# Kernel optimization log

Measured on AMD Instinct MI355X. Metric: run time of the kernel, lower is better.

The kernel has to match this reference:

```python
import jax, jax.numpy as jnp
from jax import lax
import numpy as np

B, S, D, H, L, DFF = 64, 512, 512, 8, 6, 2048
CLIP_C = 10.0
EPS = 1e-5


def setup_inputs() -> dict:
    key = jax.random.key(0)
    ks = jax.random.split(key, 16)
    sc = 0.02
    inp = {
        "x": jax.random.normal(ks[0], (B, S, D), jnp.float32),
        "mask": jnp.zeros((B, S, S), jnp.float32),
        # stacked per-layer params [L, ...]; Linear stored as (out, in) like torch
        "qkv_w": jax.random.normal(ks[1], (L, 3 * D, D), jnp.float32) * sc,
        "qkv_b": jnp.zeros((L, 3 * D), jnp.float32),
        "ln1_g": jnp.ones((L, D), jnp.float32),
        "ln1_b": jnp.zeros((L, D), jnp.float32),
        "kv_w": jax.random.normal(ks[2], (L, 2 * D, D), jnp.float32) * sc,
        "kv_b": jnp.zeros((L, 2 * D), jnp.float32),
        "ln2_g": jnp.ones((L, D), jnp.float32),
        "ln2_b": jnp.zeros((L, D), jnp.float32),
        "w1": jax.random.normal(ks[3], (L, DFF, D), jnp.float32) * sc,
        "b1": jnp.zeros((L, DFF), jnp.float32),
        "w2": jax.random.normal(ks[4], (L, D, DFF), jnp.float32) * sc,
        "b2": jnp.zeros((L, D), jnp.float32),
        "ln3_g": jnp.ones((L, D), jnp.float32),
        "ln3_b": jnp.zeros((L, D), jnp.float32),
    }
    return inp


def _ln(v, g, b):
    m = v.mean(-1, keepdims=True)
    var = ((v - m) ** 2).mean(-1, keepdims=True)
    return (v - m) * lax.rsqrt(var + EPS) * g + b


def _mha(q, k, v, mask, clip_c):
    # faithful to custom_multi_head_attn: bmm -> /sqrt(hd) -> [c*tanh] -> +mask -> softmax -> bmm
    b, sq, d = q.shape
    sk = k.shape[1]
    hd = d // H
    qh = q.reshape(b, sq, H, hd)
    kh = k.reshape(b, sk, H, hd)
    vh = v.reshape(b, sk, H, hd)
    s = jnp.einsum('bqhd,bkhd->bhqk', qh, kh) * (1.0 / float(hd) ** 0.5)
    if clip_c is not None:
        s = clip_c * jnp.tanh(s)
    if mask is not None:
        s = s + mask[:, None]  # repeat over heads
    a = jax.nn.softmax(s, axis=-1)
    return jnp.einsum('bhqk,bkhd->bqhd', a, vh).reshape(b, sq, d)


def reference(x, mask, qkv_w, qkv_b, ln1_g, ln1_b, kv_w, kv_b, ln2_g, ln2_b,
              w1, b1, w2, b2, ln3_g, ln3_b):
    def step(h, p):
        (qw, qb, g1, be1, kw, kb, g2, be2, fw1, fb1, fw2, fb2, g3, be3) = p
        # self-attention block (no FFN, no mask, no clip; note: NO out-projection,
        # matching the original which never applies out_proj_weight)
        qkv = h @ qw.T + qb
        q, k, v = jnp.split(qkv, 3, axis=-1)
        x1 = _ln(h + _mha(q, k, v, None, None), g1, be1)
        # cross-attention block: query = sa output (no q_proj), kv from original h
        kv_ = h @ kw.T + kb
        k2, v2 = jnp.split(kv_, 2, axis=-1)
        y = _ln(x1 + _mha(x1, k2, v2, mask, CLIP_C), g2, be2)
        # FFN + residual + norm (post-norm)
        ff = jax.nn.relu(y @ fw1.T + fb1) @ fw2.T + fb2
        return _ln(y + ff, g3, be3), None

    params = (qkv_w, qkv_b, ln1_g, ln1_b, kv_w, kv_b, ln2_g, ln2_b,
              w1, b1, w2, b2, ln3_g, ln3_b)
    out, _ = lax.scan(step, x, params)
    return out
```

## Files before the change

kernel.cpp:

```cpp
#include <hip/hip_runtime.h>


typedef __bf16 bf16_t;
typedef __bf16 bf16x8 __attribute__((ext_vector_type(8)));
typedef __bf16 bf16x4 __attribute__((ext_vector_type(4)));
typedef float  f32x4  __attribute__((ext_vector_type(4)));

#define NB   64
#define NS   512
#define ND   512
#define NH   8
#define NHD  64
#define NL   6
#define NDFF 2048
#define NM   (NB * NS)

__device__ __forceinline__ void gld_lds16(const void* gsrc, void* lds) {
  __builtin_amdgcn_global_load_lds((__attribute__((address_space(1))) void*)gsrc,
                                   (__attribute__((address_space(3))) void*)lds,
                                   16, 0, 0);
}

template<int N> __device__ __forceinline__ void vm_wait() {
  if constexpr (N == 0)      asm volatile("s_waitcnt vmcnt(0)" ::: "memory");
  else if constexpr (N == 3) asm volatile("s_waitcnt vmcnt(3)" ::: "memory");
}
__device__ __forceinline__ void lgkm0() {
  asm volatile("s_waitcnt lgkmcnt(0)" ::: "memory");
}

__global__ __launch_bounds__(256) void cvt_f32_bf16(const float* __restrict__ in,
                                                    bf16_t* __restrict__ out,
                                                    long n) {
  long i = ((long)blockIdx.x * 256 + threadIdx.x) * 8;
  const long stride = (long)gridDim.x * 256 * 8;
  for (; i < n; i += stride) {
    f32x4 a = *(const f32x4*)(in + i);
    f32x4 b = *(const f32x4*)(in + i + 4);
    bf16x8 o;
#pragma unroll
    for (int j = 0; j < 4; ++j) { o[j] = (bf16_t)a[j]; o[j + 4] = (bf16_t)b[j]; }
    *(bf16x8*)(out + i) = o;
  }
}

template<bool RELU, bool BIAS_ROW>
__global__ __launch_bounds__(512, 2) void gemm64(const bf16_t* __restrict__ Ap,
                                                 const bf16_t* __restrict__ Wp,
                                                 const float* __restrict__ bias,
                                                 bf16_t* __restrict__ Cout,
                                                 int Nn, int Kk) {
  __shared__ __attribute__((aligned(16))) bf16_t As[2][128 * 32];
  __shared__ __attribute__((aligned(16))) bf16_t Bs[2][256 * 32];
  const int tid = threadIdx.x;
  const int l   = tid & 63;
  const int w   = tid >> 6;
  const int wr  = w >> 2;
  const int wc  = w & 3;
  const int l15 = l & 15, lg = l >> 4;

  const int nn   = Nn >> 8;
  const int nwg  = gridDim.x;
  const int flat = blockIdx.x;
  const int wgid = (nwg & 7) ? flat : (flat & 7) * (nwg >> 3) + (flat >> 3);
  const int m0 = (wgid / nn) * 128;
  const int n0 = (wgid % nn) * 256;

  const int srow = tid >> 2;
  const int sg   = (tid & 3) ^ (srow & 3);

  auto stA = [&](int bf_, int kc) {
    gld_lds16(Ap + (size_t)(m0 + srow) * Kk + kc + sg * 8,
              &As[bf_][(w * 16) * 32]);
  };
  auto stB = [&](int bf_, int p, int kc) {
    gld_lds16(Wp + (size_t)(n0 + p * 128 + srow) * Kk + kc + sg * 8,
              &Bs[bf_][(p * 128 + w * 16) * 32]);
  };
  auto stage = [&](int kt, int bf_) {
    const int kc = kt * 32;
    stA(bf_, kc); stB(bf_, 0, kc); stB(bf_, 1, kc);
  };
  auto ldA = [&](int bf_, int mi) -> bf16x8 {
    const int row = wr * 64 + mi * 16 + l15;
    return *(const bf16x8*)&As[bf_][row * 32 + ((lg ^ (row & 3)) * 8)];
  };
  auto ldB = [&](int bf_, int ni) -> bf16x8 {
    const int row = wc * 64 + ni * 16 + l15;
    return *(const bf16x8*)&Bs[bf_][row * 32 + ((lg ^ (row & 3)) * 8)];
  };

  f32x4 acc[4][4];
#pragma unroll
  for (int i = 0; i < 4; ++i)
#pragma unroll
    for (int j = 0; j < 4; ++j) acc[i][j] = (f32x4){0.f, 0.f, 0.f, 0.f};

  const int KT = Kk >> 5;
  stage(0, 0);
  stage(1, 1);

  for (int kt = 0; kt < KT; ++kt) {
    const int buf = kt & 1;
    if (kt + 1 < KT) vm_wait<3>(); else vm_wait<0>();
    __builtin_amdgcn_s_barrier();

    bf16x8 af[4], bfr[4];
#pragma unroll
    for (int i = 0; i < 4; ++i) { af[i] = ldA(buf, i); bfr[i] = ldB(buf, i); }
    __builtin_amdgcn_s_setprio(1);
#pragma unroll
    for (int mi = 0; mi < 4; ++mi)
#pragma unroll
      for (int ni = 0; ni < 4; ++ni)
        acc[mi][ni] = __builtin_amdgcn_mfma_f32_16x16x32_bf16(af[mi], bfr[ni], acc[mi][ni], 0, 0, 0);
    __builtin_amdgcn_s_setprio(0);

    lgkm0();
    __builtin_amdgcn_s_barrier();
    if (kt + 2 < KT) stage(kt + 2, buf);
  }

#pragma unroll
  for (int mi = 0; mi < 4; ++mi)
#pragma unroll
    for (int ni = 0; ni < 4; ++ni) {
      const int col = n0 + wc * 64 + ni * 16 + l15;
      const float bc = BIAS_ROW ? 0.f : bias[col];
#pragma unroll
      for (int r = 0; r < 4; ++r) {
        const int rowi = m0 + wr * 64 + mi * 16 + lg * 4 + r;
        float v = acc[mi][ni][r] + (BIAS_ROW ? bias[rowi] : bc);
        if (RELU) v = fmaxf(v, 0.f);
        Cout[(size_t)rowi * Nn + col] = (bf16_t)v;
      }
    }
}

template<int CROSS, bool M16>
__global__ __launch_bounds__(256, 2) void attn5(const bf16_t* __restrict__ Q,
                                                const bf16_t* __restrict__ K,
                                                const bf16_t* __restrict__ Vt,
                                                const void* __restrict__ maskp,
                                                bf16_t* __restrict__ O,
                                                int qstride, int kstride, int vstride) {
  __shared__ __attribute__((aligned(16))) bf16_t k_s[2][64 * 64];
  __shared__ __attribute__((aligned(16))) bf16_t v_s[2][64 * 64];
  __shared__ __attribute__((aligned(16))) bf16_t p_s[64 * 64];

  const int tid = threadIdx.x;
  const int l   = tid & 63;
  const int w   = tid >> 6;
  const int bid = blockIdx.x;
  const int h   = bid & 7;
  const int qt  = (bid >> 3) & 7;
  const int b   = bid >> 6;
  const int h64 = h * NHD;
  const int l15 = l & 15, lg = l >> 4;

  const int qglob = qt * 64 + w * 16 + l15;

  auto stageK = [&](int kt, int buf) {
#pragma unroll
    for (int i = 0; i < 2; ++i) {
      const int r  = i * 32 + (tid >> 3);
      const int c8 = (tid & 7) ^ (r & 7);
      gld_lds16(K + (size_t)(b * NS + kt * 64 + r) * kstride + h64 + c8 * 8,
                &k_s[buf][(i * 32 + w * 8) * 64]);
    }
  };
  auto stageV = [&](int kt, int buf) {
#pragma unroll
    for (int i = 0; i < 2; ++i) {
      const int d = i * 32 + (tid >> 3);
      const int g = (tid & 7) ^ (d & 7);
      gld_lds16(Vt + (size_t)(h64 + d) * vstride + b * NS + kt * 64 + g * 8,
                &v_s[buf][(i * 32 + w * 8) * 64]);
    }
  };

  stageK(0, 0); stageV(0, 0);

  bf16x8 qf[2];
#pragma unroll
  for (int c = 0; c < 2; ++c)
    qf[c] = *(const bf16x8*)(Q + (size_t)(b * NS + qglob) * qstride + h64 + c * 32 + lg * 8);

  bf16x4 mk16[2][4];
  f32x4  mkf[2][4];
  if (CROSS) {
#pragma unroll
    for (int nt = 0; nt < 4; ++nt) {
      if (M16) mk16[0][nt] = *(const bf16x4*)((const bf16_t*)maskp
                              + (size_t)(b * NS + qglob) * NS + nt * 16 + lg * 4);
      else     mkf[0][nt]  = *(const f32x4*)((const float*)maskp
                              + (size_t)(b * NS + qglob) * NS + nt * 16 + lg * 4);
    }
  }

  float m_run = -3e38f, l_run = 0.f;
  const f32x4 zz = {0.f, 0.f, 0.f, 0.f};
  f32x4 oacc[4] = {zz, zz, zz, zz};

#pragma unroll
  for (int kt = 0; kt < 8; ++kt) {
    const int buf = kt & 1;
    __syncthreads();
    if (kt < 7) {
      stageK(kt + 1, buf ^ 1);
      stageV(kt + 1, buf ^ 1);
      if (CROSS) {
#pragma unroll
        for (int nt = 0; nt < 4; ++nt) {
          if (M16) mk16[buf ^ 1][nt] = *(const bf16x4*)((const bf16_t*)maskp
                     + (size_t)(b * NS + qglob) * NS + (kt + 1) * 64 + nt * 16 + lg * 4);
          else     mkf[buf ^ 1][nt]  = *(const f32x4*)((const float*)maskp
                     + (size_t)(b * NS + qglob) * NS + (kt + 1) * 64 + nt * 16 + lg * 4);
        }
      }
    }

    f32x4 s[4];
    __builtin_amdgcn_s_setprio(1);
#pragma unroll
    for (int nt = 0; nt < 4; ++nt) {
      const int row = nt * 16 + l15;
      bf16x8 ka0 = *(const bf16x8*)((const char*)k_s[buf] + row * 128 + ((lg ^ (row & 7)) * 16));
      bf16x8 ka1 = *(const bf16x8*)((const char*)k_s[buf] + row * 128 + (((4 + lg) ^ (row & 7)) * 16));
      f32x4 z = zz;
      z = __builtin_amdgcn_mfma_f32_16x16x32_bf16(ka0, qf[0], z, 0, 0, 0);
      z = __builtin_amdgcn_mfma_f32_16x16x32_bf16(ka1, qf[1], z, 0, 0, 0);
      s[nt] = z;
    }
    __builtin_amdgcn_s_setprio(0);

    float tmax = -3e38f;
#pragma unroll
    for (int nt = 0; nt < 4; ++nt) {
      f32x4 v = s[nt] * 0.125f;
      if (CROSS) {
#pragma unroll
        for (int r = 0; r < 4; ++r) {
          const float e2 = __expf(2.f * v[r]);
          const float mkv = M16 ? (float)mk16[buf][nt][r] : mkf[buf][nt][r];
          v[r] = 10.f - 20.f * __builtin_amdgcn_rcpf(e2 + 1.f) + mkv;
        }
      }
      s[nt] = v;
#pragma unroll
      for (int r = 0; r < 4; ++r) tmax = fmaxf(tmax, v[r]);
    }
    tmax = fmaxf(tmax, __shfl_xor(tmax, 16, 64));
    tmax = fmaxf(tmax, __shfl_xor(tmax, 32, 64));
    const float m_new = fmaxf(m_run, tmax);
    const float f = __expf(m_run - m_new);
    float fq[4];
#pragma unroll
    for (int r = 0; r < 4; ++r) fq[r] = __shfl(f, lg * 4 + r, 64);
#pragma unroll
    for (int dt = 0; dt < 4; ++dt)
#pragma unroll
      for (int r = 0; r < 4; ++r) oacc[dt][r] *= fq[r];

    float ts = 0.f;
#pragma unroll
    for (int nt = 0; nt < 4; ++nt) {
      f32x4 v = s[nt];
#pragma unroll
      for (int r = 0; r < 4; ++r) { const float e = __expf(v[r] - m_new); ts += e; v[r] = e; }
      s[nt] = v;
    }
    l_run = l_run * f + ts;
    m_run = m_new;

    const int prow = w * 16 + l15;
#pragma unroll
    for (int nt = 0; nt < 4; ++nt) {
      bf16x4 pk;
#pragma unroll
      for (int r = 0; r < 4; ++r) pk[r] = (bf16_t)s[nt][r];
      const int gran = (nt * 2 + (lg >> 1)) ^ (prow & 7);
      *(bf16x4*)((char*)p_s + prow * 128 + gran * 16 + (lg & 1) * 8) = pk;
    }

    __builtin_amdgcn_s_setprio(1);
#pragma unroll
    for (int ks = 0; ks < 2; ++ks) {
      const int ag = (ks * 4 + lg) ^ (prow & 7);
      bf16x8 pa = *(const bf16x8*)((const char*)p_s + prow * 128 + ag * 16);
#pragma unroll
      for (int dt = 0; dt < 4; ++dt) {
        const int vrow = dt * 16 + l15;
        const int vg   = (ks * 4 + lg) ^ (vrow & 7);
        bf16x8 vb = *(const bf16x8*)((const char*)v_s[buf] + vrow * 128 + vg * 16);
        oacc[dt] = __builtin_amdgcn_mfma_f32_16x16x32_bf16(pa, vb, oacc[dt], 0, 0, 0);
      }
    }
    __builtin_amdgcn_s_setprio(0);
  }

  l_run += __shfl_xor(l_run, 16, 64);
  l_run += __shfl_xor(l_run, 32, 64);
  const float inv = 1.f / l_run;
  float invq[4];
#pragma unroll
  for (int r = 0; r < 4; ++r) invq[r] = __shfl(inv, lg * 4 + r, 64);
#pragma unroll
  for (int dt = 0; dt < 4; ++dt)
#pragma unroll
    for (int r = 0; r < 4; ++r) {
      const size_t row = (size_t)(b * NS + qt * 64 + w * 16 + lg * 4 + r);
      O[row * ND + h64 + dt * 16 + l15] = (bf16_t)(oacc[dt][r] * invq[r]);
    }
}

template<bool A16, bool W32>
__global__ __launch_bounds__(256) void add_ln2(const void* __restrict__ Xav,
                                               const bf16_t* __restrict__ Xb,
                                               const float* __restrict__ gw,
                                               const float* __restrict__ bw,
                                               float* __restrict__ o32,
                                               bf16_t* __restrict__ o16) {
  const int l = threadIdx.x & 63;
  const size_t row  = (size_t)blockIdx.x * 4 + (threadIdx.x >> 6);
  const size_t base = row * ND + l * 8;
  f32x4 a0, a1;
  if (A16) {
    bf16x8 t = *(const bf16x8*)((const bf16_t*)Xav + base);
#pragma unroll
    for (int i = 0; i < 4; ++i) { a0[i] = (float)t[i]; a1[i] = (float)t[i + 4]; }
  } else {
    a0 = *(const f32x4*)((const float*)Xav + base);
    a1 = *(const f32x4*)((const float*)Xav + base + 4);
  }
  bf16x8 tb = *(const bf16x8*)(Xb + base);
  f32x4 b0, b1;
#pragma unroll
  for (int i = 0; i < 4; ++i) { b0[i] = (float)tb[i]; b1[i] = (float)tb[i + 4]; }
  f32x4 v0 = a0 + b0, v1 = a1 + b1;
  float s = v0[0] + v0[1] + v0[2] + v0[3] + v1[0] + v1[1] + v1[2] + v1[3];
#pragma unroll
  for (int off = 1; off < 64; off <<= 1) s += __shfl_xor(s, off, 64);
  const float mean = s * (1.f / ND);
  f32x4 d0 = v0 - mean, d1 = v1 - mean;
  float q = d0[0]*d0[0] + d0[1]*d0[1] + d0[2]*d0[2] + d0[3]*d0[3]
          + d1[0]*d1[0] + d1[1]*d1[1] + d1[2]*d1[2] + d1[3]*d1[3];
#pragma unroll
  for (int off = 1; off < 64; off <<= 1) q += __shfl_xor(q, off, 64);
  const float rstd = rsqrtf(q * (1.f / ND) + 1e-5f);
  const f32x4 g0 = *(const f32x4*)(gw + l * 8), g1 = *(const f32x4*)(gw + l * 8 + 4);
  const f32x4 h0 = *(const f32x4*)(bw + l * 8), h1 = *(const f32x4*)(bw + l * 8 + 4);
  f32x4 r0 = d0 * rstd * g0 + h0;
  f32x4 r1 = d1 * rstd * g1 + h1;
  if (W32) {
    *(f32x4*)(o32 + base)     = r0;
    *(f32x4*)(o32 + base + 4) = r1;
  } else {
    bf16x8 o;
#pragma unroll
    for (int i = 0; i < 4; ++i) { o[i] = (bf16_t)r0[i]; o[i + 4] = (bf16_t)r1[i]; }
    *(bf16x8*)(o16 + base) = o;
  }
}

extern "C" void kernel_launch(void* const* d_in, const int* in_sizes, int n_in,
                              void* d_out, int out_size, void* d_ws, size_t ws_size,
                              hipStream_t stream) {
  (void)in_sizes; (void)n_in; (void)out_size;
  const float* x     = (const float*)d_in[0];
  const float* maskp = (const float*)d_in[1];
  const float* qkvw  = (const float*)d_in[2];
  const float* qkvb  = (const float*)d_in[3];
  const float* ln1g  = (const float*)d_in[4];
  const float* ln1b  = (const float*)d_in[5];
  const float* kvw   = (const float*)d_in[6];
  const float* kvb   = (const float*)d_in[7];
  const float* ln2g  = (const float*)d_in[8];
  const float* ln2b  = (const float*)d_in[9];
  const float* w1p   = (const float*)d_in[10];
  const float* b1p   = (const float*)d_in[11];
  const float* w2p   = (const float*)d_in[12];
  const float* b2p   = (const float*)d_in[13];
  const float* ln3g  = (const float*)d_in[14];
  const float* ln3b  = (const float*)d_in[15];
  float* out = (float*)d_out;

  const size_t WALL = 40894464, WLYR = 6815744, H16B = 33554432, M16B = 33554432;
  struct Tier { int R; bool allw; };
  const Tier tiers[6] = {{32768, true}, {16384, true}, {8192, true},
                         {4096, true}, {2048, false}, {1024, false}};
  int R = 0; bool allw = false; size_t base_need = 0;
  for (int t = 0; t < 6; ++t) {
    size_t need = (tiers[t].allw ? WALL : WLYR) + H16B +
                  (size_t)tiers[t].R * 7168 + 16384;
    if (ws_size >= need) { R = tiers[t].R; allw = tiers[t].allw; base_need = need; break; }
  }
  if (R == 0) return;
  const bool m16 = (ws_size >= base_need + M16B + 256);
  const int nchunks = NM / R;
  const int CB = R / NS;
  const int MT = R / 128;

  char* p = (char*)d_ws;
  auto alloc = [&](size_t bytes) { char* r = p; p += (bytes + 255) & ~(size_t)255; return r; };
  bf16_t* WQ = (bf16_t*)alloc((allw ? NL : 1) * (size_t)1536 * ND * 2);
  bf16_t* WK = (bf16_t*)alloc((allw ? NL : 1) * (size_t)1024 * ND * 2);
  bf16_t* W1 = (bf16_t*)alloc((allw ? NL : 1) * (size_t)NDFF * ND * 2);
  bf16_t* W2 = (bf16_t*)alloc((allw ? NL : 1) * (size_t)ND * NDFF * 2);
  bf16_t* h16  = (bf16_t*)alloc((size_t)NM * ND * 2);
  bf16_t* big  = (bf16_t*)alloc((size_t)R * NDFF * 2);
  bf16_t* t16  = (bf16_t*)alloc((size_t)R * ND * 2);
  bf16_t* x116 = (bf16_t*)alloc((size_t)R * ND * 2);
  bf16_t* y16  = (bf16_t*)alloc((size_t)R * ND * 2);
  bf16_t* mask16 = m16 ? (bf16_t*)alloc(M16B) : nullptr;

  auto cvt = [&](const float* src, bf16_t* dst, long n) {
    int blocks = (int)((n / 8 + 255) / 256); if (blocks > 8192) blocks = 8192;
    hipLaunchKernelGGL(cvt_f32_bf16, dim3(blocks), dim3(256), 0, stream, src, dst, n);
  };

  cvt(x, h16, (long)NM * ND);
  if (m16) cvt(maskp, mask16, (long)NM * NS);
  if (allw) {
    cvt(qkvw, WQ, (long)NL * 1536 * ND);
    cvt(kvw,  WK, (long)NL * 1024 * ND);
    cvt(w1p,  W1, (long)NL * NDFF * ND);
    cvt(w2p,  W2, (long)NL * ND * NDFF);
  }

  for (int l = 0; l < NL; ++l) {
    const bf16_t *wq_l, *wk_l, *w1_l, *w2_l;
    if (allw) {
      wq_l = WQ + (size_t)l * 1536 * ND;
      wk_l = WK + (size_t)l * 1024 * ND;
      w1_l = W1 + (size_t)l * NDFF * ND;
      w2_l = W2 + (size_t)l * ND * NDFF;
    } else {
      cvt(qkvw + (size_t)l * 1536 * ND, WQ, (long)1536 * ND);
      cvt(kvw  + (size_t)l * 1024 * ND, WK, (long)1024 * ND);
      cvt(w1p  + (size_t)l * NDFF * ND, W1, (long)NDFF * ND);
      cvt(w2p  + (size_t)l * ND * NDFF, W2, (long)ND * NDFF);
      wq_l = WQ; wk_l = WK; w1_l = W1; w2_l = W2;
    }

    for (int c = 0; c < nchunks; ++c) {
      const size_t r0 = (size_t)c * R;
      bf16_t*       h16c  = h16 + r0 * ND;
      bf16_t* vtS = big + (size_t)R * 1024;
      bf16_t* vtC = big + (size_t)R * 512;

      hipLaunchKernelGGL(HIP_KERNEL_NAME(gemm64<false, false>), dim3(MT * 4), dim3(512), 0, stream,
                         h16c, wq_l, qkvb + l * 1536, big, 1024, 512);
      hipLaunchKernelGGL(HIP_KERNEL_NAME(gemm64<false, true>), dim3(4 * (R / 256)), dim3(512), 0, stream,
                         wq_l + (size_t)1024 * 512, h16c, qkvb + l * 1536 + 1024, vtS, R, 512);
      hipLaunchKernelGGL(HIP_KERNEL_NAME(attn5<0, false>), dim3(CB * 64), dim3(256), 0, stream,
                         big, big + 512, vtS, (const void*)nullptr, t16, 1024, 1024, R);
      if (l == 0)
        hipLaunchKernelGGL(HIP_KERNEL_NAME(add_ln2<false, false>), dim3(R / 4), dim3(256), 0, stream,
                           (const void*)(x + r0 * ND), t16, ln1g, ln1b, (float*)nullptr, x116);
      else
        hipLaunchKernelGGL(HIP_KERNEL_NAME(add_ln2<true, false>), dim3(R / 4), dim3(256), 0, stream,
                           (const void*)h16c, t16, ln1g + l * ND, ln1b + l * ND, (float*)nullptr, x116);
      hipLaunchKernelGGL(HIP_KERNEL_NAME(gemm64<false, false>), dim3(MT * 2), dim3(512), 0, stream,
                         h16c, wk_l, kvb + l * 1024, big, 512, 512);
      hipLaunchKernelGGL(HIP_KERNEL_NAME(gemm64<false, true>), dim3(4 * (R / 256)), dim3(512), 0, stream,
                         wk_l + (size_t)512 * 512, h16c, kvb + l * 1024 + 512, vtC, R, 512);
      if (m16)
        hipLaunchKernelGGL(HIP_KERNEL_NAME(attn5<1, true>), dim3(CB * 64), dim3(256), 0, stream,
                           x116, big, vtC, (const void*)(mask16 + r0 * NS), t16, 512, 512, R);
      else
        hipLaunchKernelGGL(HIP_KERNEL_NAME(attn5<1, false>), dim3(CB * 64), dim3(256), 0, stream,
                           x116, big, vtC, (const void*)(maskp + r0 * NS), t16, 512, 512, R);
      hipLaunchKernelGGL(HIP_KERNEL_NAME(add_ln2<true, false>), dim3(R / 4), dim3(256), 0, stream,
                         (const void*)x116, t16, ln2g + l * ND, ln2b + l * ND, (float*)nullptr, y16);
      hipLaunchKernelGGL(HIP_KERNEL_NAME(gemm64<true, false>), dim3(MT * 8), dim3(512), 0, stream,
                         y16, w1_l, b1p + l * NDFF, big, 2048, 512);
      hipLaunchKernelGGL(HIP_KERNEL_NAME(gemm64<false, false>), dim3(MT * 2), dim3(512), 0, stream,
                         big, w2_l, b2p + l * ND, t16, 512, 2048);
      if (l < NL - 1)
        hipLaunchKernelGGL(HIP_KERNEL_NAME(add_ln2<true, false>), dim3(R / 4), dim3(256), 0, stream,
                           (const void*)y16, t16, ln3g + l * ND, ln3b + l * ND, (float*)nullptr, h16c);
      else
        hipLaunchKernelGGL(HIP_KERNEL_NAME(add_ln2<true, true>), dim3(R / 4), dim3(256), 0, stream,
                           (const void*)y16, t16, ln3g + l * ND, ln3b + l * ND, out + r0 * ND, (bf16_t*)nullptr);
    }
  }
}
```

Measured before the change: 4.132 ms.

## Replace GEMM with 128x128 tile, K=64 stage, 4-wave kernel

Replaces the 8-wave 128x256 GEMM with a 4-wave 128x128-tile kernel that stages 64-wide K slices (8-way XOR swizzle) and issues the next stage's loads before waiting on the current one. Each wave still computes a 64x64 output block but does two MFMA k-steps per barrier pair, halving the number of barriers per K. Grids are doubled to match the smaller N tile. Per-block reuse of A drops because each A tile now feeds only 128 columns instead of 256, while occupancy may rise.

Result: faster. 3.812 ms (-7.8%).

```diff
diff --git a/kernel.cpp b/kernel.cpp
--- a/kernel.cpp
+++ b/kernel.cpp
@@ -23,7 +23,7 @@
 
 template<int N> __device__ __forceinline__ void vm_wait() {
   if constexpr (N == 0)      asm volatile("s_waitcnt vmcnt(0)" ::: "memory");
-  else if constexpr (N == 3) asm volatile("s_waitcnt vmcnt(3)" ::: "memory");
+  else if constexpr (N == 8) asm volatile("s_waitcnt vmcnt(8)" ::: "memory");
 }
 __device__ __forceinline__ void lgkm0() {
   asm volatile("s_waitcnt lgkmcnt(0)" ::: "memory");
@@ -45,49 +45,51 @@
 }
 
 template<bool RELU, bool BIAS_ROW>
-__global__ __launch_bounds__(512, 2) void gemm64(const bf16_t* __restrict__ Ap,
-                                                 const bf16_t* __restrict__ Wp,
-                                                 const float* __restrict__ bias,
-                                                 bf16_t* __restrict__ Cout,
-                                                 int Nn, int Kk) {
-  __shared__ __attribute__((aligned(16))) bf16_t As[2][128 * 32];
-  __shared__ __attribute__((aligned(16))) bf16_t Bs[2][256 * 32];
+__global__ __launch_bounds__(256) void gemm97(const bf16_t* __restrict__ Ap,
+                                              const bf16_t* __restrict__ Wp,
+                                              const float* __restrict__ bias,
+                                              bf16_t* __restrict__ Cout,
+                                              int Nn, int Kk) {
+  __shared__ __attribute__((aligned(16))) bf16_t As[2][128 * 64];
+  __shared__ __attribute__((aligned(16))) bf16_t Bs[2][128 * 64];
   const int tid = threadIdx.x;
   const int l   = tid & 63;
   const int w   = tid >> 6;
-  const int wr  = w >> 2;
-  const int wc  = w & 3;
+  const int wr  = (w >> 1) * 64;
+  const int wc  = (w & 1) * 64;
   const int l15 = l & 15, lg = l >> 4;
 
-  const int nn   = Nn >> 8;
+  const int nn   = Nn >> 7;
   const int nwg  = gridDim.x;
   const int flat = blockIdx.x;
   const int wgid = (nwg & 7) ? flat : (flat & 7) * (nwg >> 3) + (flat >> 3);
   const int m0 = (wgid / nn) * 128;
-  const int n0 = (wgid % nn) * 256;
-
-  const int srow = tid >> 2;
-  const int sg   = (tid & 3) ^ (srow & 3);
-
-  auto stA = [&](int bf_, int kc) {
-    gld_lds16(Ap + (size_t)(m0 + srow) * Kk + kc + sg * 8,
-              &As[bf_][(w * 16) * 32]);
-  };
-  auto stB = [&](int bf_, int p, int kc) {
-    gld_lds16(Wp + (size_t)(n0 + p * 128 + srow) * Kk + kc + sg * 8,
-              &Bs[bf_][(p * 128 + w * 16) * 32]);
-  };
+  const int n0 = (wgid % nn) * 128;
+
+  const int prow = w * 32 + (l >> 3);
+
   auto stage = [&](int kt, int bf_) {
-    const int kc = kt * 32;
-    stA(bf_, kc); stB(bf_, 0, kc); stB(bf_, 1, kc);
-  };
-  auto ldA = [&](int bf_, int mi) -> bf16x8 {
-    const int row = wr * 64 + mi * 16 + l15;
-    return *(const bf16x8*)&As[bf_][row * 32 + ((lg ^ (row & 3)) * 8)];
-  };
-  auto ldB = [&](int bf_, int ni) -> bf16x8 {
-    const int row = wc * 64 + ni * 16 + l15;
-    return *(const bf16x8*)&Bs[bf_][row * 32 + ((lg ^ (row & 3)) * 8)];
+    const int kc = kt * 64;
+#pragma unroll
+    for (int i = 0; i < 4; ++i) {
+      const int rA = prow + i * 8;
+      const int g  = (l & 7) ^ (rA & 7);
+      gld_lds16(Ap + (size_t)(m0 + rA) * Kk + kc + g * 8, &As[bf_][(w * 4 + i) * 512]);
+    }
+#pragma unroll
+    for (int i = 0; i < 4; ++i) {
+      const int rB = prow + i * 8;
+      const int g  = (l & 7) ^ (rB & 7);
+      gld_lds16(Wp + (size_t)(n0 + rB) * Kk + kc + g * 8, &Bs[bf_][(w * 4 + i) * 512]);
+    }
+  };
+  auto ldA = [&](int bf_, int mi, int kk) -> bf16x8 {
+    const int row = wr + mi * 16 + l15;
+    return *(const bf16x8*)&As[bf_][row * 64 + (((kk * 4 + lg) ^ (row & 7)) * 8)];
+  };
+  auto ldB = [&](int bf_, int ni, int kk) -> bf16x8 {
+    const int row = wc + ni * 16 + l15;
+    return *(const bf16x8*)&Bs[bf_][row * 64 + (((kk * 4 + lg) ^ (row & 7)) * 8)];
   };
 
   f32x4 acc[4][4];
@@ -96,40 +98,41 @@
 #pragma unroll
     for (int j = 0; j < 4; ++j) acc[i][j] = (f32x4){0.f, 0.f, 0.f, 0.f};
 
-  const int KT = Kk >> 5;
+  const int KT = Kk >> 6;
   stage(0, 0);
-  stage(1, 1);
-
+
+  int buf = 0;
   for (int kt = 0; kt < KT; ++kt) {
-    const int buf = kt & 1;
-    if (kt + 1 < KT) vm_wait<3>(); else vm_wait<0>();
+    if (kt + 1 < KT) { stage(kt + 1, buf ^ 1); vm_wait<8>(); }
+    else             vm_wait<0>();
     __builtin_amdgcn_s_barrier();
-
-    bf16x8 af[4], bfr[4];
-#pragma unroll
-    for (int i = 0; i < 4; ++i) { af[i] = ldA(buf, i); bfr[i] = ldB(buf, i); }
-    __builtin_amdgcn_s_setprio(1);
-#pragma unroll
-    for (int mi = 0; mi < 4; ++mi)
-#pragma unroll
-      for (int ni = 0; ni < 4; ++ni)
-        acc[mi][ni] = __builtin_amdgcn_mfma_f32_16x16x32_bf16(af[mi], bfr[ni], acc[mi][ni], 0, 0, 0);
-    __builtin_amdgcn_s_setprio(0);
-
+#pragma unroll
+    for (int kk = 0; kk < 2; ++kk) {
+      bf16x8 af[4], bw[4];
+#pragma unroll
+      for (int i = 0; i < 4; ++i) { af[i] = ldA(buf, i, kk); bw[i] = ldB(buf, i, kk); }
+      __builtin_amdgcn_s_setprio(1);
+#pragma unroll
+      for (int mi = 0; mi < 4; ++mi)
+#pragma unroll
+        for (int ni = 0; ni < 4; ++ni)
+          acc[mi][ni] = __builtin_amdgcn_mfma_f32_16x16x32_bf16(af[mi], bw[ni], acc[mi][ni], 0, 0, 0);
+      __builtin_amdgcn_s_setprio(0);
+    }
     lgkm0();
     __builtin_amdgcn_s_barrier();
-    if (kt + 2 < KT) stage(kt + 2, buf);
+    buf ^= 1;
   }
 
 #pragma unroll
   for (int mi = 0; mi < 4; ++mi)
 #pragma unroll
     for (int ni = 0; ni < 4; ++ni) {
-      const int col = n0 + wc * 64 + ni * 16 + l15;
+      const int col = n0 + wc + ni * 16 + l15;
       const float bc = BIAS_ROW ? 0.f : bias[col];
 #pragma unroll
       for (int r = 0; r < 4; ++r) {
-        const int rowi = m0 + wr * 64 + mi * 16 + lg * 4 + r;
+        const int rowi = m0 + wr + mi * 16 + lg * 4 + r;
         float v = acc[mi][ni][r] + (BIAS_ROW ? bias[rowi] : bc);
         if (RELU) v = fmaxf(v, 0.f);
         Cout[(size_t)rowi * Nn + col] = (bf16_t)v;
@@ -449,9 +452,9 @@
       bf16_t* vtS = big + (size_t)R * 1024;
       bf16_t* vtC = big + (size_t)R * 512;
 
-      hipLaunchKernelGGL(HIP_KERNEL_NAME(gemm64<false, false>), dim3(MT * 4), dim3(512), 0, stream,
+      hipLaunchKernelGGL(HIP_KERNEL_NAME(gemm97<false, false>), dim3(MT * 8), dim3(256), 0, stream,
                          h16c, wq_l, qkvb + l * 1536, big, 1024, 512);
-      hipLaunchKernelGGL(HIP_KERNEL_NAME(gemm64<false, true>), dim3(4 * (R / 256)), dim3(512), 0, stream,
+      hipLaunchKernelGGL(HIP_KERNEL_NAME(gemm97<false, true>), dim3(MT * 4), dim3(256), 0, stream,
                          wq_l + (size_t)1024 * 512, h16c, qkvb + l * 1536 + 1024, vtS, R, 512);
       hipLaunchKernelGGL(HIP_KERNEL_NAME(attn5<0, false>), dim3(CB * 64), dim3(256), 0, stream,
                          big, big + 512, vtS, (const void*)nullptr, t16, 1024, 1024, R);
@@ -461,9 +464,9 @@
       else
         hipLaunchKernelGGL(HIP_KERNEL_NAME(add_ln2<true, false>), dim3(R / 4), dim3(256), 0, stream,
                            (const void*)h16c, t16, ln1g + l * ND, ln1b + l * ND, (float*)nullptr, x116);
-      hipLaunchKernelGGL(HIP_KERNEL_NAME(gemm64<false, false>), dim3(MT * 2), dim3(512), 0, stream,
+      hipLaunchKernelGGL(HIP_KERNEL_NAME(gemm97<false, false>), dim3(MT * 4), dim3(256), 0, stream,
                          h16c, wk_l, kvb + l * 1024, big, 512, 512);
-      hipLaunchKernelGGL(HIP_KERNEL_NAME(gemm64<false, true>), dim3(4 * (R / 256)), dim3(512), 0, stream,
+      hipLaunchKernelGGL(HIP_KERNEL_NAME(gemm97<false, true>), dim3(MT * 4), dim3(256), 0, stream,
                          wk_l + (size_t)512 * 512, h16c, kvb + l * 1024 + 512, vtC, R, 512);
       if (m16)
         hipLaunchKernelGGL(HIP_KERNEL_NAME(attn5<1, true>), dim3(CB * 64), dim3(256), 0, stream,
@@ -473,9 +476,9 @@
                            x116, big, vtC, (const void*)(maskp + r0 * NS), t16, 512, 512, R);
       hipLaunchKernelGGL(HIP_KERNEL_NAME(add_ln2<true, false>), dim3(R / 4), dim3(256), 0, stream,
                          (const void*)x116, t16, ln2g + l * ND, ln2b + l * ND, (float*)nullptr, y16);
-      hipLaunchKernelGGL(HIP_KERNEL_NAME(gemm64<true, false>), dim3(MT * 8), dim3(512), 0, stream,
+      hipLaunchKernelGGL(HIP_KERNEL_NAME(gemm97<true, false>), dim3(MT * 16), dim3(256), 0, stream,
                          y16, w1_l, b1p + l * NDFF, big, 2048, 512);
-      hipLaunchKernelGGL(HIP_KERNEL_NAME(gemm64<false, false>), dim3(MT * 2), dim3(512), 0, stream,
+      hipLaunchKernelGGL(HIP_KERNEL_NAME(gemm97<false, false>), dim3(MT * 4), dim3(256), 0, stream,
                          big, w2_l, b2p + l * ND, t16, 512, 2048);
       if (l < NL - 1)
         hipLaunchKernelGGL(HIP_KERNEL_NAME(add_ln2<true, false>), dim3(R / 4), dim3(256), 0, stream,
```

## Switch GEMM to 4-wave 256-thread blocks with 64x128 per-wave tiles

Applied to the files above, without the earlier changes.

Replaces the 8-wave 512-thread GEMM with a 4-wave kernel where each wave computes a 64x128 output tile (32 MFMA accumulators), doubling per-wave register reuse of A fragments. The staging pipeline changes from a two-ahead prefetch issued after compute to a one-ahead prefetch issued before the wait, and the LDS swizzle uses (row>>1)&3. Fewer waves per block and more accumulator registers per thread lower occupancy and may reduce latency hiding. The prefetch overlap is also shallower.

New measurement: 4.787 ms. 1.16x slower.

```diff
diff --git a/kernel.cpp b/kernel.cpp
--- a/kernel.cpp
+++ b/kernel.cpp
@@ -23,7 +23,7 @@
 
 template<int N> __device__ __forceinline__ void vm_wait() {
   if constexpr (N == 0)      asm volatile("s_waitcnt vmcnt(0)" ::: "memory");
-  else if constexpr (N == 3) asm volatile("s_waitcnt vmcnt(3)" ::: "memory");
+  else if constexpr (N == 6) asm volatile("s_waitcnt vmcnt(6)" ::: "memory");
 }
 __device__ __forceinline__ void lgkm0() {
   asm volatile("s_waitcnt lgkmcnt(0)" ::: "memory");
@@ -45,18 +45,18 @@
 }
 
 template<bool RELU, bool BIAS_ROW>
-__global__ __launch_bounds__(512, 2) void gemm64(const bf16_t* __restrict__ Ap,
-                                                 const bf16_t* __restrict__ Wp,
-                                                 const float* __restrict__ bias,
-                                                 bf16_t* __restrict__ Cout,
-                                                 int Nn, int Kk) {
+__global__ __launch_bounds__(256) void gemmW(const bf16_t* __restrict__ Ap,
+                                             const bf16_t* __restrict__ Wp,
+                                             const float* __restrict__ bias,
+                                             bf16_t* __restrict__ Cout,
+                                             int Nn, int Kk) {
   __shared__ __attribute__((aligned(16))) bf16_t As[2][128 * 32];
   __shared__ __attribute__((aligned(16))) bf16_t Bs[2][256 * 32];
   const int tid = threadIdx.x;
   const int l   = tid & 63;
   const int w   = tid >> 6;
-  const int wr  = w >> 2;
-  const int wc  = w & 3;
+  const int wr  = w >> 1;
+  const int wc  = w & 1;
   const int l15 = l & 15, lg = l >> 4;
 
   const int nn   = Nn >> 8;
@@ -66,66 +66,70 @@
   const int m0 = (wgid / nn) * 128;
   const int n0 = (wgid % nn) * 256;
 
-  const int srow = tid >> 2;
-  const int sg   = (tid & 3) ^ (srow & 3);
-
-  auto stA = [&](int bf_, int kc) {
-    gld_lds16(Ap + (size_t)(m0 + srow) * Kk + kc + sg * 8,
-              &As[bf_][(w * 16) * 32]);
+  auto stA = [&](int bf_, int p, int kc) {
+    const int row = p * 64 + (tid >> 2);
+    const int g   = (tid & 3) ^ ((row >> 1) & 3);
+    gld_lds16(Ap + (size_t)(m0 + row) * Kk + kc + g * 8,
+              &As[bf_][(p * 64 + w * 16) * 32]);
   };
   auto stB = [&](int bf_, int p, int kc) {
-    gld_lds16(Wp + (size_t)(n0 + p * 128 + srow) * Kk + kc + sg * 8,
-              &Bs[bf_][(p * 128 + w * 16) * 32]);
+    const int row = p * 64 + (tid >> 2);
+    const int g   = (tid & 3) ^ ((row >> 1) & 3);
+    gld_lds16(Wp + (size_t)(n0 + row) * Kk + kc + g * 8,
+              &Bs[bf_][(p * 64 + w * 16) * 32]);
   };
   auto stage = [&](int kt, int bf_) {
     const int kc = kt * 32;
-    stA(bf_, kc); stB(bf_, 0, kc); stB(bf_, 1, kc);
+    stA(bf_, 0, kc); stA(bf_, 1, kc);
+    stB(bf_, 0, kc); stB(bf_, 1, kc); stB(bf_, 2, kc); stB(bf_, 3, kc);
   };
   auto ldA = [&](int bf_, int mi) -> bf16x8 {
     const int row = wr * 64 + mi * 16 + l15;
-    return *(const bf16x8*)&As[bf_][row * 32 + ((lg ^ (row & 3)) * 8)];
+    return *(const bf16x8*)&As[bf_][row * 32 + ((lg ^ ((row >> 1) & 3)) * 8)];
   };
   auto ldB = [&](int bf_, int ni) -> bf16x8 {
-    const int row = wc * 64 + ni * 16 + l15;
-    return *(const bf16x8*)&Bs[bf_][row * 32 + ((lg ^ (row & 3)) * 8)];
-  };
-
-  f32x4 acc[4][4];
+    const int row = wc * 128 + ni * 16 + l15;
+    return *(const bf16x8*)&Bs[bf_][row * 32 + ((lg ^ ((row >> 1) & 3)) * 8)];
+  };
+
+  f32x4 acc[4][8];
 #pragma unroll
   for (int i = 0; i < 4; ++i)
 #pragma unroll
-    for (int j = 0; j < 4; ++j) acc[i][j] = (f32x4){0.f, 0.f, 0.f, 0.f};
+    for (int j = 0; j < 8; ++j) acc[i][j] = (f32x4){0.f, 0.f, 0.f, 0.f};
 
   const int KT = Kk >> 5;
   stage(0, 0);
-  stage(1, 1);
-
+
+  int buf = 0;
   for (int kt = 0; kt < KT; ++kt) {
-    const int buf = kt & 1;
-    if (kt + 1 < KT) vm_wait<3>(); else vm_wait<0>();
+    if (kt + 1 < KT) { stage(kt + 1, buf ^ 1); vm_wait<6>(); }
+    else             vm_wait<0>();
     __builtin_amdgcn_s_barrier();
 
-    bf16x8 af[4], bfr[4];
-#pragma unroll
-    for (int i = 0; i < 4; ++i) { af[i] = ldA(buf, i); bfr[i] = ldB(buf, i); }
+    bf16x8 af[4], bfr[8];
+#pragma unroll
+    for (int i = 0; i < 4; ++i) af[i] = ldA(buf, i);
+#pragma unroll
+    for (int i = 0; i < 8; ++i) bfr[i] = ldB(buf, i);
     __builtin_amdgcn_s_setprio(1);
 #pragma unroll
     for (int mi = 0; mi < 4; ++mi)
 #pragma unroll
-      for (int ni = 0; ni < 4; ++ni)
+      for (int ni = 0; ni < 8; ++ni)
         acc[mi][ni] = __builtin_amdgcn_mfma_f32_16x16x32_bf16(af[mi], bfr[ni], acc[mi][ni], 0, 0, 0);
     __builtin_amdgcn_s_setprio(0);
 
     lgkm0();
     __builtin_amdgcn_s_barrier();
-    if (kt + 2 < KT) stage(kt + 2, buf);
+    buf ^= 1;
   }
 
 #pragma unroll
   for (int mi = 0; mi < 4; ++mi)
 #pragma unroll
-    for (int ni = 0; ni < 4; ++ni) {
-      const int col = n0 + wc * 64 + ni * 16 + l15;
+    for (int ni = 0; ni < 8; ++ni) {
+      const int col = n0 + wc * 128 + ni * 16 + l15;
       const float bc = BIAS_ROW ? 0.f : bias[col];
 #pragma unroll
       for (int r = 0; r < 4; ++r) {
@@ -449,9 +453,9 @@
       bf16_t* vtS = big + (size_t)R * 1024;
       bf16_t* vtC = big + (size_t)R * 512;
 
-      hipLaunchKernelGGL(HIP_KERNEL_NAME(gemm64<false, false>), dim3(MT * 4), dim3(512), 0, stream,
+      hipLaunchKernelGGL(HIP_KERNEL_NAME(gemmW<false, false>), dim3(MT * 4), dim3(256), 0, stream,
                          h16c, wq_l, qkvb + l * 1536, big, 1024, 512);
-      hipLaunchKernelGGL(HIP_KERNEL_NAME(gemm64<false, true>), dim3(4 * (R / 256)), dim3(512), 0, stream,
+      hipLaunchKernelGGL(HIP_KERNEL_NAME(gemmW<false, true>), dim3(MT * 2), dim3(256), 0, stream,
                          wq_l + (size_t)1024 * 512, h16c, qkvb + l * 1536 + 1024, vtS, R, 512);
       hipLaunchKernelGGL(HIP_KERNEL_NAME(attn5<0, false>), dim3(CB * 64), dim3(256), 0, stream,
                          big, big + 512, vtS, (const void*)nullptr, t16, 1024, 1024, R);
@@ -461,9 +465,9 @@
       else
         hipLaunchKernelGGL(HIP_KERNEL_NAME(add_ln2<true, false>), dim3(R / 4), dim3(256), 0, stream,
                            (const void*)h16c, t16, ln1g + l * ND, ln1b + l * ND, (float*)nullptr, x116);
-      hipLaunchKernelGGL(HIP_KERNEL_NAME(gemm64<false, false>), dim3(MT * 2), dim3(512), 0, stream,
+      hipLaunchKernelGGL(HIP_KERNEL_NAME(gemmW<false, false>), dim3(MT * 2), dim3(256), 0, stream,
                          h16c, wk_l, kvb + l * 1024, big, 512, 512);
-      hipLaunchKernelGGL(HIP_KERNEL_NAME(gemm64<false, true>), dim3(4 * (R / 256)), dim3(512), 0, stream,
+      hipLaunchKernelGGL(HIP_KERNEL_NAME(gemmW<false, true>), dim3(MT * 2), dim3(256), 0, stream,
                          wk_l + (size_t)512 * 512, h16c, kvb + l * 1024 + 512, vtC, R, 512);
       if (m16)
         hipLaunchKernelGGL(HIP_KERNEL_NAME(attn5<1, true>), dim3(CB * 64), dim3(256), 0, stream,
@@ -473,9 +477,9 @@
                            x116, big, vtC, (const void*)(maskp + r0 * NS), t16, 512, 512, R);
       hipLaunchKernelGGL(HIP_KERNEL_NAME(add_ln2<true, false>), dim3(R / 4), dim3(256), 0, stream,
                          (const void*)x116, t16, ln2g + l * ND, ln2b + l * ND, (float*)nullptr, y16);
-      hipLaunchKernelGGL(HIP_KERNEL_NAME(gemm64<true, false>), dim3(MT * 8), dim3(512), 0, stream,
+      hipLaunchKernelGGL(HIP_KERNEL_NAME(gemmW<true, false>), dim3(MT * 8), dim3(256), 0, stream,
                          y16, w1_l, b1p + l * NDFF, big, 2048, 512);
-      hipLaunchKernelGGL(HIP_KERNEL_NAME(gemm64<false, false>), dim3(MT * 2), dim3(512), 0, stream,
+      hipLaunchKernelGGL(HIP_KERNEL_NAME(gemmW<false, false>), dim3(MT * 2), dim3(256), 0, stream,
                          big, w2_l, b2p + l * ND, t16, 512, 2048);
       if (l < NL - 1)
         hipLaunchKernelGGL(HIP_KERNEL_NAME(add_ln2<true, false>), dim3(R / 4), dim3(256), 0, stream,
```
